# Kernel tuning notes

Measured on AMD Instinct MI355X. Metric: run time of the kernel, lower is better.

Reference implementation:

```python
import jax, jax.numpy as jnp
import numpy as np

B, N, C, G, K = 4, 6000, 91, 32, 100
IMG = 800.0
SCORE_TH = 0.05
NMS_TH = 0.5
MATCH_TH = 0.5
MIN_SIZE = 0.01
BBOX_CLIP = float(np.log(1000.0 / 16.0))
WX, WY, WW, WH = 10.0, 10.0, 5.0, 5.0


def _make_boxes(key, shape_prefix):
    k1, k2 = jax.random.split(key)
    xy = jax.random.uniform(k1, shape_prefix + (2,), minval=0.0, maxval=IMG - 130.0)
    wh = jax.random.uniform(k2, shape_prefix + (2,), minval=8.0, maxval=128.0)
    return jnp.concatenate([xy, xy + wh], axis=-1)


def setup_inputs() -> dict:
    key = jax.random.key(0)
    k1, k2, k3, k4, k5 = jax.random.split(key, 5)
    return {
        "class_logits": 2.0 * jax.random.normal(k1, (B * N, C), dtype=jnp.float32),
        "box_regression": jax.random.normal(k2, (B * N, C * 4), dtype=jnp.float32),
        "proposals": _make_boxes(k3, (B, N)),
        "gt_boxes": _make_boxes(k4, (B, G)),
        "gt_labels": jax.random.randint(k5, (B, G), 1, C),
    }


def _box_iou(a, b):
    # a [G,4], b [N,4] -> [G,N]
    area_a = (a[:, 2] - a[:, 0]) * (a[:, 3] - a[:, 1])
    area_b = (b[:, 2] - b[:, 0]) * (b[:, 3] - b[:, 1])
    lt = jnp.maximum(a[:, None, :2], b[None, :, :2])
    rb = jnp.minimum(a[:, None, 2:], b[None, :, 2:])
    wh = jnp.clip(rb - lt, 0.0)
    inter = wh[..., 0] * wh[..., 1]
    return inter / (area_a[:, None] + area_b[None, :] - inter)


def _decode(rel, props):
    # torchvision BoxCoder.decode; rel [N,C,4], props [N,4]
    w = props[:, 2] - props[:, 0]
    h = props[:, 3] - props[:, 1]
    cx = props[:, 0] + 0.5 * w
    cy = props[:, 1] + 0.5 * h
    dx = rel[..., 0] / WX
    dy = rel[..., 1] / WY
    dw = jnp.minimum(rel[..., 2] / WW, BBOX_CLIP)
    dh = jnp.minimum(rel[..., 3] / WH, BBOX_CLIP)
    pcx = dx * w[:, None] + cx[:, None]
    pcy = dy * h[:, None] + cy[:, None]
    pw = jnp.exp(dw) * w[:, None]
    ph = jnp.exp(dh) * h[:, None]
    return jnp.stack([pcx - 0.5 * pw, pcy - 0.5 * ph, pcx + 0.5 * pw, pcy + 0.5 * ph], axis=-1)


def _image(logits, reg, props, gtb, gtl):
    # --- assign_targets_to_proposals (Matcher, low=high=0.5, no low-quality matches) ---
    iou = _box_iou(gtb, props)                      # [G, N]
    best = iou.max(axis=0)
    mi = jnp.argmax(iou, axis=0)
    matched = jnp.where(best >= MATCH_TH, mi, -1)   # -1 == BELOW_LOW_THRESHOLD
    assigned = jnp.where(matched >= 0, gtl[jnp.clip(matched, 0)], 0)

    # --- postprocess_detections ---
    scores = jax.nn.softmax(logits, axis=-1)[:, 1:].reshape(-1)                       # [N*(C-1)]
    boxes = jnp.clip(_decode(reg.reshape(N, C, 4), props)[:, 1:], 0.0, IMG)
    boxes = boxes.reshape(-1, 4)                                                      # [N*(C-1),4]
    labels = jnp.tile(jnp.arange(1, C), N)                                            # [N*(C-1)]
    ws = boxes[:, 2] - boxes[:, 0]
    hs = boxes[:, 3] - boxes[:, 1]
    valid = (scores > SCORE_TH) & (ws >= MIN_SIZE) & (hs >= MIN_SIZE)
    s0 = jnp.where(valid, scores, -jnp.inf)
    # batched_nms trick: offset boxes by label so cross-class IoU is 0
    off = boxes + (labels.astype(boxes.dtype) * (IMG + 1.0))[:, None]
    off_area = (off[:, 2] - off[:, 0]) * (off[:, 3] - off[:, 1])

    def step(s, _):
        i = jnp.argmax(s)
        sc = s[i]
        b = off[i]
        lt = jnp.maximum(off[:, :2], b[:2])
        rb = jnp.minimum(off[:, 2:], b[2:])
        wh = jnp.clip(rb - lt, 0.0)
        inter = wh[:, 0] * wh[:, 1]
        iou_all = inter / (off_area + (b[2] - b[0]) * (b[3] - b[1]) - inter)
        s = jnp.where(iou_all > NMS_TH, -jnp.inf, s)  # suppress (includes self)
        ok = jnp.isfinite(sc)
        ob = jnp.where(ok, boxes[i], 0.0)
        osc = jnp.where(ok, sc, 0.0)
        ol = jnp.where(ok, labels[i], -1)
        return s, (ob, osc, ol)

    _, (kb, ksc, kl) = jax.lax.scan(step, s0, None, length=K)
    return kb, ksc, kl, assigned, matched


def reference(class_logits, box_regression, proposals, gt_boxes, gt_labels):
    logits = class_logits.reshape(B, N, C)
    reg = box_regression.reshape(B, N, C * 4)
    kb, ksc, kl, assigned, matched = jax.vmap(_image)(logits, reg, proposals, gt_boxes, gt_labels)
    dets = jnp.concatenate([kb, ksc[..., None]], axis=-1)  # [B, K, 5]
    return dets, kl, assigned, matched
```

## Files before the change

kernel.cpp:

```cpp
#include <hip/hip_runtime.h>
#include <math.h>

#define NB 4
#define NN 6000
#define NC 91
#define NG 32
#define NK 100
#define NCLS (NC - 1)
#define NBUC (NB * NCLS)
#define PMAX 512
#define MATW 256
#define MPB 4096
#define RS_BLOCKS 6000

#define SCORE_TH 0.05f
#define NMS_TH 0.5f
#define MATCH_TH 0.5f
#define MIN_SIZE 0.01f
#define BBOX_CLIP 4.135166556742356f
#define C_SUP 0.5000000298023223876953125

#define CFENCE() asm volatile("" ::: "memory")

__device__ __forceinline__ bool decode_one(
    const float* __restrict__ reg, const float* __restrict__ props,
    float l, float m, float s0, int row, int c, float out[5])
{
    float score = __fdiv_rn(expf(__fsub_rn(l, m)), s0);

    const float4 p = *reinterpret_cast<const float4*>(props + (size_t)row * 4);
    float w  = __fsub_rn(p.z, p.x);
    float h  = __fsub_rn(p.w, p.y);
    float cx = __fadd_rn(p.x, __fmul_rn(0.5f, w));
    float cy = __fadd_rn(p.y, __fmul_rn(0.5f, h));

    const float4 r4 = *reinterpret_cast<const float4*>(
        reg + (size_t)row * (NC * 4) + (size_t)c * 4);
    float dx = __fdiv_rn(r4.x, 10.0f);
    float dy = __fdiv_rn(r4.y, 10.0f);
    float dw = fminf(__fdiv_rn(r4.z, 5.0f), BBOX_CLIP);
    float dh = fminf(__fdiv_rn(r4.w, 5.0f), BBOX_CLIP);

    float pcx = __fadd_rn(__fmul_rn(dx, w), cx);
    float pcy = __fadd_rn(__fmul_rn(dy, h), cy);
    float pw  = __fmul_rn(expf(dw), w);
    float ph  = __fmul_rn(expf(dh), h);

    float x1 = __fsub_rn(pcx, __fmul_rn(0.5f, pw));
    float y1 = __fsub_rn(pcy, __fmul_rn(0.5f, ph));
    float x2 = __fadd_rn(pcx, __fmul_rn(0.5f, pw));
    float y2 = __fadd_rn(pcy, __fmul_rn(0.5f, ph));
    x1 = fminf(fmaxf(x1, 0.0f), 800.0f);
    y1 = fminf(fmaxf(y1, 0.0f), 800.0f);
    x2 = fminf(fmaxf(x2, 0.0f), 800.0f);
    y2 = fminf(fmaxf(y2, 0.0f), 800.0f);

    out[0] = score; out[1] = x1; out[2] = y1; out[3] = x2; out[4] = y2;
    float ws_ = __fsub_rn(x2, x1);
    float hs_ = __fsub_rn(y2, y1);
    return (score > SCORE_TH) && (ws_ >= MIN_SIZE) && (hs_ >= MIN_SIZE);
}

__global__ __launch_bounds__(256) void fused_kernel(
    const float* __restrict__ logits, const float* __restrict__ reg,
    const float* __restrict__ props, const float* __restrict__ gtb,
    const int* __restrict__ gtl,
    float* __restrict__ out_assigned, float* __restrict__ out_matched,
    unsigned char* __restrict__ flags, float* __restrict__ ent)
{
    int bid = blockIdx.x;
    if (bid < RS_BLOCKS) {
        int wid = threadIdx.x >> 6, lane = threadIdx.x & 63;
        int row = bid * 4 + wid;
        const float* rp = logits + (size_t)row * NC;
        float l0 = rp[lane];
        float l1 = (lane < NC - 64) ? rp[64 + lane] : -INFINITY;
        float m = fmaxf(fmaxf(-INFINITY, l0), l1);
        for (int o = 32; o; o >>= 1) m = fmaxf(m, __shfl_down(m, o));
        m = __shfl(m, 0);
        float s = __fadd_rn(__fadd_rn(0.0f, expf(__fsub_rn(l0, m))),
                            expf(__fsub_rn(l1, m)));
        for (int o = 32; o; o >>= 1) s = __fadd_rn(s, __shfl_down(s, o));
        float s0 = __shfl(s, 0);
        float thr = __fadd_rn(m, logf(__fmul_rn(0.04f, s0)));

        int b = row / NN;
        int nprop = row - b * NN;

        if (lane >= 1 && l0 > thr) {
            float o[5];
            if (decode_one(reg, props, l0, m, s0, row, lane, o)) {
                int g = b * NCLS + (lane - 1);
                size_t sl = (size_t)g * NN + nprop;
                float* e = ent + sl * 8;
                *reinterpret_cast<float4*>(e) =
                    make_float4(o[1], o[2], o[3], o[4]);
                *reinterpret_cast<float2*>(e + 4) =
                    make_float2(o[0], (float)(nprop * NCLS + (lane - 1)));
                flags[sl] = 1;
            }
        }
        if (lane < NC - 64 && l1 > thr) {
            float o[5];
            int c = lane + 64;
            if (decode_one(reg, props, l1, m, s0, row, c, o)) {
                int g = b * NCLS + (c - 1);
                size_t sl = (size_t)g * NN + nprop;
                float* e = ent + sl * 8;
                *reinterpret_cast<float4*>(e) =
                    make_float4(o[1], o[2], o[3], o[4]);
                *reinterpret_cast<float2*>(e + 4) =
                    make_float2(o[0], (float)(nprop * NCLS + (c - 1)));
                flags[sl] = 1;
            }
        }
    } else {
        int t = (bid - RS_BLOCKS) * 256 + threadIdx.x;
        if (t >= NB * NN) return;
        int b = t / NN;
        const float4 p = *reinterpret_cast<const float4*>(props + (size_t)t * 4);
        float parea = __fmul_rn(__fsub_rn(p.z, p.x), __fsub_rn(p.w, p.y));
        float best = -1.0f; int bi = -1;
        for (int g = 0; g < NG; ++g) {
            const float4 q = *reinterpret_cast<const float4*>(gtb + ((size_t)b * NG + g) * 4);
            float garea = __fmul_rn(__fsub_rn(q.z, q.x), __fsub_rn(q.w, q.y));
            float ltx = fmaxf(q.x, p.x), lty = fmaxf(q.y, p.y);
            float rbx = fminf(q.z, p.z), rby = fminf(q.w, p.w);
            float wx = fmaxf(__fsub_rn(rbx, ltx), 0.0f);
            float wy = fmaxf(__fsub_rn(rby, lty), 0.0f);
            float inter = __fmul_rn(wx, wy);
            float iou = __fdiv_rn(inter, __fsub_rn(__fadd_rn(garea, parea), inter));
            if (iou > best) { best = iou; bi = g; }
        }
        int matched = (best >= MATCH_TH) ? bi : -1;
        int assigned = (matched >= 0) ? gtl[b * NG + matched] : 0;
        out_matched[t]  = (float)matched;
        out_assigned[t] = (float)assigned;
    }
}

__device__ void nms_glb_sparse(int g, const unsigned char* __restrict__ F,
                               float* __restrict__ E, float tb, float cls,
                               float* __restrict__ selbuf, int* __restrict__ selcnt)
{
    int lane = threadIdx.x & 63;
    int kout = 0;
    for (int k = 0; k < NK; ++k) {
        float bv = -INFINITY, boi = INFINITY; int bi = -1;
        for (int i = lane; i < NN; i += 64) {
            if (!F[i]) continue;
            float v = E[(size_t)i * 8 + 4], oi = E[(size_t)i * 8 + 5];
            if (v > bv || (v == bv && oi < boi)) { bv = v; boi = oi; bi = i; }
        }
        int wl = lane;
        for (int o = 1; o < 64; o <<= 1) {
            float v2 = __shfl_xor(bv, o); float o2 = __shfl_xor(boi, o);
            int l2 = __shfl_xor(wl, o);
            bool bt = (v2 > bv) || (v2 == bv && o2 < boi);
            bv = bt ? v2 : bv; boi = bt ? o2 : boi; wl = bt ? l2 : wl;
        }
        if (bv == -INFINITY) break;
        int wi = __shfl(bi, wl);
        float sx1 = E[(size_t)wi * 8 + 0], sy1 = E[(size_t)wi * 8 + 1];
        float sx2 = E[(size_t)wi * 8 + 2], sy2 = E[(size_t)wi * 8 + 3];
        if (lane == wl) {
            float* so = selbuf + ((size_t)g * NK + k) * 8;
            so[0] = bv; so[1] = sx1; so[2] = sy1; so[3] = sx2; so[4] = sy2;
            so[5] = cls; so[6] = boi; so[7] = 0.0f;
        }
        float bx1 = __fadd_rn(sx1, tb), by1 = __fadd_rn(sy1, tb);
        float bx2 = __fadd_rn(sx2, tb), by2 = __fadd_rn(sy2, tb);
        float sar = __fmul_rn(__fsub_rn(bx2, bx1), __fsub_rn(by2, by1));
        for (int i = lane; i < NN; i += 64) {
            if (!F[i]) continue;
            float v = E[(size_t)i * 8 + 4];
            if (v == -INFINITY) continue;
            float ox1 = __fadd_rn(E[(size_t)i * 8 + 0], tb);
            float oy1 = __fadd_rn(E[(size_t)i * 8 + 1], tb);
            float ox2 = __fadd_rn(E[(size_t)i * 8 + 2], tb);
            float oy2 = __fadd_rn(E[(size_t)i * 8 + 3], tb);
            float oar = __fmul_rn(__fsub_rn(ox2, ox1), __fsub_rn(oy2, oy1));
            float ltx = fmaxf(ox1, bx1), lty = fmaxf(oy1, by1);
            float rbx = fminf(ox2, bx2), rby = fminf(oy2, by2);
            float wx = fmaxf(__fsub_rn(rbx, ltx), 0.0f);
            float wy = fmaxf(__fsub_rn(rby, lty), 0.0f);
            float inter = __fmul_rn(wx, wy);
            float den = __fsub_rn(__fadd_rn(oar, sar), inter);
            if ((double)inter > C_SUP * (double)den) E[(size_t)i * 8 + 4] = -INFINITY;
        }
        kout = k + 1;
    }
    if (lane == 0) selcnt[g] = kout;
}

template <int CAP>
__device__ __forceinline__ float selN(const float a[CAP], int j) {
    float r = a[0];
#pragma unroll
    for (int i = 1; i < CAP; ++i) r = (j == i) ? a[i] : r;
    return r;
}
__device__ __forceinline__ float rdlane(float v, int l) {
    return __uint_as_float(
        (unsigned)__builtin_amdgcn_readlane((int)__float_as_uint(v), l));
}
__device__ __forceinline__ unsigned long long rdlane64(unsigned long long v, int l) {
    unsigned lo = (unsigned)__builtin_amdgcn_readlane((int)(unsigned)v, l);
    unsigned hi = (unsigned)__builtin_amdgcn_readlane((int)(unsigned)(v >> 32), l);
    return ((unsigned long long)hi << 32) | lo;
}

template <int CAP>
__device__ __forceinline__ int sweep_reg(
    int lane, int n, float tb,
    const float* sx1, const float* sy1, const float* sx2, const float* sy2,
    int* acc)
{
    float ox1[CAP], oy1[CAP], ox2[CAP], oy2[CAP], oar[CAP];
    unsigned alive = 0;
#pragma unroll
    for (int j = 0; j < CAP; ++j) {
        int sidx = lane * CAP + j;
        if (sidx < n) {
            float a  = __fadd_rn(sx1[sidx], tb);
            float b_ = __fadd_rn(sy1[sidx], tb);
            float c_ = __fadd_rn(sx2[sidx], tb);
            float d_ = __fadd_rn(sy2[sidx], tb);
            ox1[j] = a; oy1[j] = b_; ox2[j] = c_; oy2[j] = d_;
            oar[j] = __fmul_rn(__fsub_rn(c_, a), __fsub_rn(d_, b_));
            alive |= 1u << j;
        } else {
            ox1[j] = 0.f; oy1[j] = 0.f; ox2[j] = 0.f; oy2[j] = 0.f; oar[j] = 0.f;
        }
    }
    int kout = 0;
    while (kout < NK) {
        unsigned long long bal = __ballot(alive != 0u);
        if (!bal) break;
        int fl = (int)__ffsll(bal) - 1;
        unsigned am = (unsigned)__builtin_amdgcn_readlane((int)alive, fl);
        int js = __ffs(am) - 1;
        float bx1 = rdlane(selN<CAP>(ox1, js), fl);
        float by1 = rdlane(selN<CAP>(oy1, js), fl);
        float bx2 = rdlane(selN<CAP>(ox2, js), fl);
        float by2 = rdlane(selN<CAP>(oy2, js), fl);
        float bar = rdlane(selN<CAP>(oar, js), fl);
        if (lane == 0) acc[kout] = fl * CAP + js;
        kout++;
        unsigned kill = 0;
#pragma unroll
        for (int j = 0; j < CAP; ++j) {
            float ltx = fmaxf(ox1[j], bx1), lty = fmaxf(oy1[j], by1);
            float rbx = fminf(ox2[j], bx2), rby = fminf(oy2[j], by2);
            float wx = fmaxf(__fsub_rn(rbx, ltx), 0.0f);
            float wy = fmaxf(__fsub_rn(rby, lty), 0.0f);
            float inter = __fmul_rn(wx, wy);
            float den = __fsub_rn(__fadd_rn(oar[j], bar), inter);
            if ((double)inter > C_SUP * (double)den) kill |= 1u << j;
        }
        alive &= ~kill;
    }
    return kout;
}

__global__ __launch_bounds__(512) void bucket_nms_kernel(
    const unsigned char* __restrict__ flags,
    float* __restrict__ entries,
    float* __restrict__ selbuf, int* __restrict__ selcnt)
{
    int g = blockIdx.x;
    int tid = threadIdx.x;
    float* E = entries + (size_t)g * NN * 8;
    const unsigned char* F = flags + (size_t)g * NN;
    float cls = (float)(g % NCLS + 1);
    float tb = __fmul_rn(cls, 801.0f);

    __shared__ int sidx[PMAX];
    __shared__ int s_n;
    __shared__ unsigned skhi[PMAX], sklo[PMAX];
    __shared__ int sperm[PMAX];
    __shared__ float sx1[PMAX], sy1[PMAX], sx2[PMAX], sy2[PMAX];
    __shared__ unsigned long long dmask[MATW * 4];
    __shared__ int acc[NK];
    __shared__ int s_kout, s_fb;

    if (tid == 0) s_n = 0;
    __syncthreads();
    for (int i = tid; i < NN; i += 512) {
        if (F[i]) {
            int p = atomicAdd(&s_n, 1);
            if (p < PMAX) sidx[p] = i;
        }
    }
    __syncthreads();
    int ntot = s_n;
    if (ntot == 0) { if (tid == 0) selcnt[g] = 0; return; }
    if (ntot > PMAX) {
        if (tid < 64) nms_glb_sparse(g, F, E, tb, cls, selbuf, selcnt);
        return;
    }
    int n = ntot;

    int P = 64; while (P < n) P <<= 1;

    for (int i = tid; i < P; i += 512) {
        if (i < n) {
            const float2 kv = *reinterpret_cast<const float2*>(
                E + (size_t)sidx[i] * 8 + 4);
            skhi[i] = __float_as_uint(kv.x);
            sklo[i] = ~((unsigned)kv.y);
        } else { skhi[i] = 0u; sklo[i] = 0u; }
        sperm[i] = i;
    }
    __syncthreads();
    for (int k = 2; k <= P; k <<= 1) {
        for (int j = k >> 1; j > 0; j >>= 1) {
            bool cross = (j >= 128);
            if (cross) __syncthreads();
            for (int t = tid; t < (P >> 1); t += 512) {
                int i = ((t & ~(j - 1)) << 1) | (t & (j - 1));
                int l = i | j;
                unsigned ah = skhi[i], al = sklo[i], ch = skhi[l], cl_ = sklo[l];
                bool alt = (ah < ch) || (ah == ch && al < cl_);
                bool agt = (ah > ch) || (ah == ch && al > cl_);
                bool sw = ((i & k) == 0) ? alt : agt;
                if (sw) {
                    skhi[i] = ch; sklo[i] = cl_; skhi[l] = ah; sklo[l] = al;
                    int tp = sperm[i]; sperm[i] = sperm[l]; sperm[l] = tp;
                }
            }
            if (cross) __syncthreads();
            else CFENCE();
        }
    }
    __syncthreads();
    for (int i = tid; i < n; i += 512) {
        const float4 v = *reinterpret_cast<const float4*>(
            E + (size_t)sidx[sperm[i]] * 8);
        sx1[i] = v.x; sy1[i] = v.y; sx2[i] = v.z; sy2[i] = v.w;
    }
    __syncthreads();

    int W = (n < MATW) ? n : MATW;
    int nchunk = (W + 63) >> 6;
    int wv = tid >> 6, lane = tid & 63;

    float jx1[4], jy1[4], jx2[4], jy2[4], jar[4];
#pragma unroll
    for (int c = 0; c < 4; ++c) {
        int j = c * 64 + lane;
        if (j < W) {
            float a  = __fadd_rn(sx1[j], tb);
            float b_ = __fadd_rn(sy1[j], tb);
            float c_ = __fadd_rn(sx2[j], tb);
            float d_ = __fadd_rn(sy2[j], tb);
            jx1[c] = a; jy1[c] = b_; jx2[c] = c_; jy2[c] = d_;
            jar[c] = __fmul_rn(__fsub_rn(c_, a), __fsub_rn(d_, b_));
        } else {
            jx1[c] = 0.f; jy1[c] = 0.f; jx2[c] = 0.f; jy2[c] = 0.f; jar[c] = 0.f;
        }
    }
    {
        int i0 = wv;
        float nx1 = 0.f, ny1 = 0.f, nx2 = 0.f, ny2 = 0.f;
        if (i0 < W) { nx1 = sx1[i0]; ny1 = sy1[i0]; nx2 = sx2[i0]; ny2 = sy2[i0]; }
        for (int i = i0; i < W; i += 8) {
            float rx1 = nx1, ry1 = ny1, rx2 = nx2, ry2 = ny2;
            int ni = i + 8;
            if (ni < W) { nx1 = sx1[ni]; ny1 = sy1[ni]; nx2 = sx2[ni]; ny2 = sy2[ni]; }
            float bx1 = __fadd_rn(rx1, tb), by1 = __fadd_rn(ry1, tb);
            float bx2 = __fadd_rn(rx2, tb), by2 = __fadd_rn(ry2, tb);
            float bar = __fmul_rn(__fsub_rn(bx2, bx1), __fsub_rn(by2, by1));
            int ic = i >> 6;
#pragma unroll
            for (int c = 0; c < 4; ++c) {
                if (c >= ic && c < nchunk) {
                    bool jv = (c * 64 + lane) < W;
                    float ltx = fmaxf(jx1[c], bx1), lty = fmaxf(jy1[c], by1);
                    float rbx = fminf(jx2[c], bx2), rby = fminf(jy2[c], by2);
                    float wx = fmaxf(__fsub_rn(rbx, ltx), 0.0f);
                    float wy = fmaxf(__fsub_rn(rby, lty), 0.0f);
                    float inter = __fmul_rn(wx, wy);
                    float den = __fsub_rn(__fadd_rn(jar[c], bar), inter);
                    bool sup = jv && ((double)inter > C_SUP * (double)den);
                    unsigned long long w64 = __ballot(sup);
                    if (lane == 0) dmask[i * 4 + c] = w64;
                }
            }
        }
    }
    __syncthreads();

    if (tid < 64) {
        unsigned long long a0 = 0, a1 = 0, a2 = 0, a3 = 0;
        {
            int rem = W;
            a0 = (rem >= 64) ? ~0ull : ((rem > 0) ? ((1ull << rem) - 1) : 0); rem -= 64;
            a1 = (rem >= 64) ? ~0ull : ((rem > 0) ? ((1ull << rem) - 1) : 0); rem -= 64;
            a2 = (rem >= 64) ? ~0ull : ((rem > 0) ? ((1ull << rem) - 1) : 0); rem -= 64;
            a3 = (rem >= 64) ? ~0ull : ((rem > 0) ? ((1ull << rem) - 1) : 0);
        }
        int kout = 0;
        while (kout < NK) {
            int cand;
            if      (a0) cand = (int)__ffsll(a0) - 1;
            else if (a1) cand = 64  + (int)__ffsll(a1) - 1;
            else if (a2) cand = 128 + (int)__ffsll(a2) - 1;
            else if (a3) cand = 192 + (int)__ffsll(a3) - 1;
            else break;
            if (lane == 0) acc[kout] = cand;
            kout++;
            unsigned long long mrow = (lane < 4) ? dmask[cand * 4 + lane] : 0ull;
            a0 &= ~rdlane64(mrow, 0);
            a1 &= ~rdlane64(mrow, 1);
            a2 &= ~rdlane64(mrow, 2);
            a3 &= ~rdlane64(mrow, 3);
        }
        if (lane == 0) {
            s_kout = kout;
            s_fb = (kout < NK && n > W) ? 1 : 0;
        }
    }
    __syncthreads();

    if (s_fb) {
        if (tid < 64) {
            int kout = sweep_reg<8>(lane, n, tb, sx1, sy1, sx2, sy2, acc);
            if (lane == 0) s_kout = kout;
        }
        __syncthreads();
    }

    int kc = s_kout;
    if (tid == 0) selcnt[g] = kc;
    for (int k = tid; k < kc; k += 512) {
        int cand = acc[k];
        float* so = selbuf + ((size_t)g * NK + k) * 8;
        so[0] = __uint_as_float(skhi[cand]);
        so[1] = sx1[cand]; so[2] = sy1[cand];
        so[3] = sx2[cand]; so[4] = sy2[cand];
        so[5] = cls; so[6] = (float)(~sklo[cand]); so[7] = 0.0f;
    }
}

__global__ __launch_bounds__(512) void merge_kernel(
    const float* __restrict__ selbuf, const int* __restrict__ selcnt,
    float* __restrict__ out_dets, float* __restrict__ out_kl)
{
    int b = blockIdx.x, tid = threadIdx.x;
    __shared__ int scnt[NCLS], soff[NCLS + 1];
    __shared__ unsigned akhi[512], aklo[512];
    __shared__ unsigned bkhi[MPB], bklo[MPB], bpay[MPB];
    __shared__ int s_T, s_cntA;
    __shared__ unsigned s_LBhi, s_LBlo;

    if (tid < NCLS) scnt[tid] = selcnt[b * NCLS + tid];
    if (tid == 0) s_T = 0;
    __syncthreads();
    if (tid == 0) {
        int a = 0, ca = 0;
        for (int c = 0; c < NCLS; ++c) {
            soff[c] = a; a += scnt[c];
            ca += (scnt[c] < 4 ? scnt[c] : 4);
        }
        soff[NCLS] = a; s_cntA = ca;
    }
    __syncthreads();
    int tot = soff[NCLS];

    if (tot == 0) {
        for (int z = tid; z < NK * 5; z += 512) out_dets[(size_t)b * NK * 5 + z] = 0.0f;
        for (int z = tid; z < NK; z += 512)     out_kl[(size_t)b * NK + z] = -1.0f;
        return;
    }

    {
        unsigned kh = 0u, kl = 0u;
        if (tid < NCLS * 4) {
            int c = tid >> 2, i = tid & 3;
            if (i < scnt[c]) {
                const float* e = selbuf + ((size_t)(b * NCLS + c) * NK + i) * 8;
                kh = __float_as_uint(e[0]); kl = ~((unsigned)e[6]);
            }
        }
        akhi[tid] = kh; aklo[tid] = kl;
    }
    __syncthreads();
    for (int k = 2; k <= 512; k <<= 1) {
        for (int j = k >> 1; j > 0; j >>= 1) {
            bool cross = (j >= 128);
            if (cross) __syncthreads();
            if (tid < 256) {
                int t = tid;
                int i = ((t & ~(j - 1)) << 1) | (t & (j - 1));
                int l = i | j;
                unsigned ah = akhi[i], al = aklo[i], ch = akhi[l], cl_ = aklo[l];
                bool alt = (ah < ch) || (ah == ch && al < cl_);
                bool agt = (ah > ch) || (ah == ch && al > cl_);
                bool sw = ((i & k) == 0) ? alt : agt;
                if (sw) {
                    akhi[i] = ch; aklo[i] = cl_; akhi[l] = ah; aklo[l] = al;
                }
            }
            if (cross) __syncthreads();
            else CFENCE();
        }
    }
    __syncthreads();
    if (tid == 0) {
        if (s_cntA >= NK) { s_LBhi = akhi[NK - 1]; s_LBlo = aklo[NK - 1]; }
        else              { s_LBhi = 0u;           s_LBlo = 0u; }
    }
    __syncthreads();
    unsigned LBhi = s_LBhi, LBlo = s_LBlo;

    for (int flat = tid; flat < tot; flat += 512) {
        int lo = 0, hi = NCLS - 1;
        while (lo < hi) { int mid = (lo + hi + 1) >> 1;
                          if (soff[mid] <= flat) lo = mid; else hi = mid - 1; }
        int c = lo, i = flat - soff[c];
        const float* e = selbuf + ((size_t)(b * NCLS + c) * NK + i) * 8;
        unsigned kh = __float_as_uint(e[0]), kl = ~((unsigned)e[6]);
        bool ge = (kh > LBhi) || (kh == LBhi && kl >= LBlo);
        if (ge) {
            int pos = atomicAdd(&s_T, 1);
            if (pos < MPB) { bkhi[pos] = kh; bklo[pos] = kl;
                             bpay[pos] = (unsigned)((c << 7) | i); }
        }
    }
    __syncthreads();
    int T = s_T;

    if (T > MPB) {
        if (tid >= 64) return;
        int lane = tid;
        int g0 = b * NCLS + lane;
        int g1 = (lane < NCLS - 64) ? g0 + 64 : -1;
        int c0 = scnt[lane];
        int c1 = (g1 >= 0) ? scnt[lane + 64] : 0;
        int p0 = 0, p1 = 0;
        unsigned long long k0c = 0, k1c = 0;
        if (p0 < c0) { const float* h = selbuf + ((size_t)g0 * NK) * 8;
            k0c = ((unsigned long long)__float_as_uint(h[0]) << 32) | (unsigned long long)(~(unsigned)h[6]); }
        if (g1 >= 0 && p1 < c1) { const float* h = selbuf + ((size_t)g1 * NK) * 8;
            k1c = ((unsigned long long)__float_as_uint(h[0]) << 32) | (unsigned long long)(~(unsigned)h[6]); }
        for (int k = 0; k < NK; ++k) {
            bool t1 = (k1c > k0c);
            unsigned long long bk = t1 ? k1c : k0c;
            int bslot = t1 ? (lane + 64) : lane;
            for (int o = 1; o < 64; o <<= 1) {
                unsigned long long k2 = __shfl_xor(bk, o);
                int b2 = __shfl_xor(bslot, o);
                if (k2 > bk) { bk = k2; bslot = b2; }
            }
            if (bk == 0ull) {
                for (int z = k * 5 + lane; z < NK * 5; z += 64)
                    out_dets[(size_t)b * NK * 5 + z] = 0.0f;
                for (int z = k + lane; z < NK; z += 64)
                    out_kl[(size_t)b * NK + z] = -1.0f;
                return;
            }
            int owner = bslot & 63;
            if (lane == owner) {
                bool isA = (bslot < 64);
                int gg = isA ? g0 : g1;
                int pp = isA ? p0 : p1;
                const float* e = selbuf + ((size_t)gg * NK + pp) * 8;
                size_t o = ((size_t)b * NK + k) * 5;
                out_dets[o + 0] = e[1]; out_dets[o + 1] = e[2];
                out_dets[o + 2] = e[3]; out_dets[o + 3] = e[4];
                out_dets[o + 4] = e[0];
                out_kl[(size_t)b * NK + k] = e[5];
                if (isA) {
                    p0++; k0c = 0;
                    if (p0 < c0) { const float* h = selbuf + ((size_t)g0 * NK + p0) * 8;
                        k0c = ((unsigned long long)__float_as_uint(h[0]) << 32) | (unsigned long long)(~(unsigned)h[6]); }
                } else {
                    p1++; k1c = 0;
                    if (p1 < c1) { const float* h = selbuf + ((size_t)g1 * NK + p1) * 8;
                        k1c = ((unsigned long long)__float_as_uint(h[0]) << 32) | (unsigned long long)(~(unsigned)h[6]); }
                }
            }
        }
        return;
    }

    int P = 128; while (P < T) P <<= 1;
    for (int i = T + tid; i < P; i += 512) { bkhi[i] = 0u; bklo[i] = 0u; bpay[i] = 0u; }
    __syncthreads();
    for (int k = 2; k <= P; k <<= 1) {
        for (int j = k >> 1; j > 0; j >>= 1) {
            bool cross = (j >= 128);
            if (cross) __syncthreads();
            for (int t = tid; t < (P >> 1); t += 512) {
                int i = ((t & ~(j - 1)) << 1) | (t & (j - 1));
                int l = i | j;
                unsigned ah = bkhi[i], al = bklo[i], ch = bkhi[l], cl_ = bklo[l];
                bool alt = (ah < ch) || (ah == ch && al < cl_);
                bool agt = (ah > ch) || (ah == ch && al > cl_);
                bool sw = ((i & k) == 0) ? alt : agt;
                if (sw) {
                    bkhi[i] = ch; bklo[i] = cl_; bkhi[l] = ah; bklo[l] = al;
                    unsigned tp = bpay[i]; bpay[i] = bpay[l]; bpay[l] = tp;
                }
            }
            if (cross) __syncthreads();
            else CFENCE();
        }
    }
    __syncthreads();
    int kc = (T < NK) ? T : NK;
    for (int k = tid; k < NK; k += 512) {
        size_t o = ((size_t)b * NK + k) * 5;
        if (k < kc) {
            unsigned pay = bpay[k];
            int c = (int)(pay >> 7), p = (int)(pay & 127);
            const float* e = selbuf + ((size_t)(b * NCLS + c) * NK + p) * 8;
            out_dets[o + 0] = e[1]; out_dets[o + 1] = e[2];
            out_dets[o + 2] = e[3]; out_dets[o + 3] = e[4];
            out_dets[o + 4] = e[0];
            out_kl[(size_t)b * NK + k] = e[5];
        } else {
            out_dets[o + 0] = 0.0f; out_dets[o + 1] = 0.0f;
            out_dets[o + 2] = 0.0f; out_dets[o + 3] = 0.0f;
            out_dets[o + 4] = 0.0f;
            out_kl[(size_t)b * NK + k] = -1.0f;
        }
    }
}

extern "C" void kernel_launch(void* const* d_in, const int* in_sizes, int n_in,
                              void* d_out, int out_size, void* d_ws, size_t ws_size,
                              hipStream_t stream) {
    const float* logits = (const float*)d_in[0];
    const float* reg    = (const float*)d_in[1];
    const float* props  = (const float*)d_in[2];
    const float* gtb    = (const float*)d_in[3];
    const int*   gtl    = (const int*)d_in[4];

    float* out          = (float*)d_out;
    float* out_dets     = out;
    float* out_kl       = out + NB * NK * 5;
    float* out_assigned = out_kl + NB * NK;
    float* out_matched  = out_assigned + NB * NN;

    char* ws = (char*)d_ws;
    int*   selcnt  = (int*)(ws + 0);
    float* selbuf  = (float*)(ws + 65536);
    unsigned char* flags = (unsigned char*)(ws + 2097152);
    float* entries = (float*)(ws + 8388608);

    hipMemsetAsync(flags, 0, (size_t)NBUC * NN, stream);
    const int MATCH_BLOCKS = (NB * NN + 255) / 256;
    fused_kernel<<<RS_BLOCKS + MATCH_BLOCKS, 256, 0, stream>>>(
        logits, reg, props, gtb, gtl, out_assigned, out_matched,
        flags, entries);
    bucket_nms_kernel<<<NBUC, 512, 0, stream>>>(
        flags, entries, selbuf, selcnt);
    merge_kernel<<<NB, 512, 0, stream>>>(selbuf, selcnt, out_dets, out_kl);
}
```

Measured before the change: 119.3 us.

## Replace per-candidate byte flags with atomic 64-bit bitmasks per bucket

Candidate-presence flags move from one byte per proposal to 64-bit mask words per class bucket, set with atomicOr in the fused kernel. The memset shrinks from about 2.1 MB to about 276 KB. The NMS kernel compacts candidates with popcount and a prefix sum over 94 words instead of scanning 6000 bytes with a shared atomic counter. This also makes candidate order deterministic. In exchange, every surviving candidate now issues a global 64-bit atomic, and the prefix sum runs serially on a single thread.

```diff
diff --git a/kernel.cpp b/kernel.cpp
--- a/kernel.cpp
+++ b/kernel.cpp
@@ -8,6 +8,8 @@
 #define NK 100
 #define NCLS (NC - 1)
 #define NBUC (NB * NCLS)
+#define NWRD 94
+#define NWRD_P 96
 #define PMAX 512
 #define MATW 256
 #define MPB 4096
@@ -66,7 +68,7 @@
     const float* __restrict__ props, const float* __restrict__ gtb,
     const int* __restrict__ gtl,
     float* __restrict__ out_assigned, float* __restrict__ out_matched,
-    unsigned char* __restrict__ flags, float* __restrict__ ent)
+    unsigned long long* __restrict__ masks, float* __restrict__ ent)
 {
     int bid = blockIdx.x;
     if (bid < RS_BLOCKS) {
@@ -91,13 +93,13 @@
             float o[5];
             if (decode_one(reg, props, l0, m, s0, row, lane, o)) {
                 int g = b * NCLS + (lane - 1);
-                size_t sl = (size_t)g * NN + nprop;
-                float* e = ent + sl * 8;
+                float* e = ent + ((size_t)g * NN + nprop) * 8;
                 *reinterpret_cast<float4*>(e) =
                     make_float4(o[1], o[2], o[3], o[4]);
                 *reinterpret_cast<float2*>(e + 4) =
                     make_float2(o[0], (float)(nprop * NCLS + (lane - 1)));
-                flags[sl] = 1;
+                atomicOr(&masks[(size_t)g * NWRD_P + (nprop >> 6)],
+                         1ull << (nprop & 63));
             }
         }
         if (lane < NC - 64 && l1 > thr) {
@@ -105,13 +107,13 @@
             int c = lane + 64;
             if (decode_one(reg, props, l1, m, s0, row, c, o)) {
                 int g = b * NCLS + (c - 1);
-                size_t sl = (size_t)g * NN + nprop;
-                float* e = ent + sl * 8;
+                float* e = ent + ((size_t)g * NN + nprop) * 8;
                 *reinterpret_cast<float4*>(e) =
                     make_float4(o[1], o[2], o[3], o[4]);
                 *reinterpret_cast<float2*>(e + 4) =
                     make_float2(o[0], (float)(nprop * NCLS + (c - 1)));
-                flags[sl] = 1;
+                atomicOr(&masks[(size_t)g * NWRD_P + (nprop >> 6)],
+                         1ull << (nprop & 63));
             }
         }
     } else {
@@ -139,7 +141,7 @@
     }
 }
 
-__device__ void nms_glb_sparse(int g, const unsigned char* __restrict__ F,
+__device__ void nms_glb_sparse(int g, const unsigned long long* __restrict__ M,
                                float* __restrict__ E, float tb, float cls,
                                float* __restrict__ selbuf, int* __restrict__ selcnt)
 {
@@ -148,7 +150,7 @@
     for (int k = 0; k < NK; ++k) {
         float bv = -INFINITY, boi = INFINITY; int bi = -1;
         for (int i = lane; i < NN; i += 64) {
-            if (!F[i]) continue;
+            if (!((M[i >> 6] >> (i & 63)) & 1ull)) continue;
             float v = E[(size_t)i * 8 + 4], oi = E[(size_t)i * 8 + 5];
             if (v > bv || (v == bv && oi < boi)) { bv = v; boi = oi; bi = i; }
         }
@@ -172,7 +174,7 @@
         float bx2 = __fadd_rn(sx2, tb), by2 = __fadd_rn(sy2, tb);
         float sar = __fmul_rn(__fsub_rn(bx2, bx1), __fsub_rn(by2, by1));
         for (int i = lane; i < NN; i += 64) {
-            if (!F[i]) continue;
+            if (!((M[i >> 6] >> (i & 63)) & 1ull)) continue;
             float v = E[(size_t)i * 8 + 4];
             if (v == -INFINITY) continue;
             float ox1 = __fadd_rn(E[(size_t)i * 8 + 0], tb);
@@ -264,19 +266,19 @@
 }
 
 __global__ __launch_bounds__(512) void bucket_nms_kernel(
-    const unsigned char* __restrict__ flags,
+    const unsigned long long* __restrict__ masks,
     float* __restrict__ entries,
     float* __restrict__ selbuf, int* __restrict__ selcnt)
 {
     int g = blockIdx.x;
     int tid = threadIdx.x;
     float* E = entries + (size_t)g * NN * 8;
-    const unsigned char* F = flags + (size_t)g * NN;
+    const unsigned long long* M = masks + (size_t)g * NWRD_P;
     float cls = (float)(g % NCLS + 1);
     float tb = __fmul_rn(cls, 801.0f);
 
     __shared__ int sidx[PMAX];
-    __shared__ int s_n;
+    __shared__ int woff[NWRD + 1];
     __shared__ unsigned skhi[PMAX], sklo[PMAX];
     __shared__ int sperm[PMAX];
     __shared__ float sx1[PMAX], sy1[PMAX], sx2[PMAX], sy2[PMAX];
@@ -284,22 +286,31 @@
     __shared__ int acc[NK];
     __shared__ int s_kout, s_fb;
 
-    if (tid == 0) s_n = 0;
-    __syncthreads();
-    for (int i = tid; i < NN; i += 512) {
-        if (F[i]) {
-            int p = atomicAdd(&s_n, 1);
-            if (p < PMAX) sidx[p] = i;
-        }
-    }
-    __syncthreads();
-    int ntot = s_n;
-    if (ntot == 0) { if (tid == 0) selcnt[g] = 0; return; }
-    if (ntot > PMAX) {
-        if (tid < 64) nms_glb_sparse(g, F, E, tb, cls, selbuf, selcnt);
+    unsigned long long myw = (tid < NWRD) ? M[tid] : 0ull;
+    if (tid < NWRD) woff[tid] = __popcll(myw);
+    __syncthreads();
+    if (tid == 0) {
+        int a = 0;
+        for (int w = 0; w < NWRD; ++w) { int c = woff[w]; woff[w] = a; a += c; }
+        woff[NWRD] = a;
+    }
+    __syncthreads();
+    int n = woff[NWRD];
+    if (n == 0) { if (tid == 0) selcnt[g] = 0; return; }
+    if (n > PMAX) {
+        if (tid < 64) nms_glb_sparse(g, M, E, tb, cls, selbuf, selcnt);
         return;
     }
-    int n = ntot;
+    if (tid < NWRD) {
+        unsigned long long m = myw;
+        int base = woff[tid], r = 0;
+        while (m) {
+            int b = (int)__ffsll(m) - 1;
+            sidx[base + r] = tid * 64 + b;
+            r++; m &= m - 1;
+        }
+    }
+    __syncthreads();
 
     int P = 64; while (P < n) P <<= 1;
 
@@ -647,15 +658,17 @@
     char* ws = (char*)d_ws;
     int*   selcnt  = (int*)(ws + 0);
     float* selbuf  = (float*)(ws + 65536);
-    unsigned char* flags = (unsigned char*)(ws + 2097152);
+    unsigned long long* masks =
+        (unsigned long long*)(ws + 2097152);
     float* entries = (float*)(ws + 8388608);
 
-    hipMemsetAsync(flags, 0, (size_t)NBUC * NN, stream);
+    hipMemsetAsync(masks, 0, (size_t)NBUC * NWRD_P * sizeof(unsigned long long),
+                   stream);
     const int MATCH_BLOCKS = (NB * NN + 255) / 256;
     fused_kernel<<<RS_BLOCKS + MATCH_BLOCKS, 256, 0, stream>>>(
         logits, reg, props, gtb, gtl, out_assigned, out_matched,
-        flags, entries);
+        masks, entries);
     bucket_nms_kernel<<<NBUC, 512, 0, stream>>>(
-        flags, entries, selbuf, selcnt);
+        masks, entries, selbuf, selcnt);
     merge_kernel<<<NB, 512, 0, stream>>>(selbuf, selcnt, out_dets, out_kl);
 }
```

After: 115.4 us, median of 4. -3.2%, faster.
